# Performance work log

Measured on AMD Instinct MI355X. Metric: run time of the kernel, lower is better.

Reference implementation:

```python
import jax, jax.numpy as jnp
import numpy as np

N, E, F_IN, H, C = 50000, 800000, 50, 128, 121


def setup_inputs() -> dict:
    key = jax.random.key(0)
    ks = jax.random.split(key, 16)
    s = 0.05
    inp = {
        'x': jax.random.normal(ks[0], (N, F_IN), jnp.float32),
        'edge_index': jax.random.randint(ks[1], (2, E), 0, N, jnp.int64),
        'TRAIN': 0,
        'W1': jax.random.normal(ks[2], (F_IN, H), jnp.float32) * s,
        'b1': jnp.zeros((H,), jnp.float32),
        'W2': jax.random.normal(ks[3], (H, H), jnp.float32) * s,
        'b2': jnp.zeros((H,), jnp.float32),
        'W3': jax.random.normal(ks[4], (H, H), jnp.float32) * s,
        'b3': jnp.zeros((H,), jnp.float32),
        'fcW1': jax.random.normal(ks[5], (H, H), jnp.float32) * s,
        'fcb1': jnp.zeros((H,), jnp.float32),
        'fcW2': jax.random.normal(ks[6], (H, H), jnp.float32) * s,
        'fcb2': jnp.zeros((H,), jnp.float32),
        'fcW3': jax.random.normal(ks[7], (H, C), jnp.float32) * s,
        'fcb3': jnp.zeros((C,), jnp.float32),
    }
    return inp


def gcn_conv(x, W, b, src, dst, n):
    # PyG GCNConv: h = x @ W; symmetric norm with self-loops; aggregate at dst.
    h = x @ W
    deg = jax.ops.segment_sum(jnp.ones(src.shape[0], h.dtype), dst, num_segments=n) + 1.0
    dinv = jax.lax.rsqrt(deg)  # deg^{-1/2}, self-loop included
    norm = dinv[src] * dinv[dst]  # [E]
    agg = jax.ops.segment_sum(h[src] * norm[:, None], dst, num_segments=n)
    agg = agg + h * (dinv * dinv)[:, None]  # self-loop contribution
    return agg + b


def reference(x, edge_index, TRAIN, W1, b1, W2, b2, W3, b3, fcW1, fcb1, fcW2, fcb2, fcW3, fcb3):
    src, dst = edge_index[0], edge_index[1]
    n = x.shape[0]
    y = jax.nn.relu(gcn_conv(x, W1, b1, src, dst, n))
    y = jax.nn.relu(gcn_conv(y, W2, b2, src, dst, n))
    y = jax.nn.relu(gcn_conv(y, W3, b3, src, dst, n))
    y = jax.nn.relu(y @ fcW1 + fcb1)
    y = jax.nn.relu(y @ fcW2 + fcb2)
    y = y @ fcW3 + fcb3
    return y
```

## Files before the change

### kernel.cpp

```cpp
#include <hip/hip_runtime.h>

#define SCAN_CHUNK 2048

typedef short s16x8 __attribute__((ext_vector_type(8)));
typedef float f32x4 __attribute__((ext_vector_type(4)));

__device__ inline ushort f2b(float f) {
  uint u = __float_as_uint(f);
  return (ushort)((u + 0x7fffu + ((u >> 16) & 1u)) >> 16);
}
__device__ inline float b2f(uint h) { return __uint_as_float(h << 16); }

__global__ __launch_bounds__(256) void zero_kernel(int4* __restrict__ p, int n4) {
  int i = blockIdx.x * 256 + threadIdx.x;
  if (i < n4) p[i] = make_int4(0, 0, 0, 0);
}

__global__ __launch_bounds__(256) void convert_hist_kernel(const void* __restrict__ ei,
                                                           int* __restrict__ src,
                                                           int* __restrict__ dst,
                                                           int* __restrict__ degi, int E) {
  __shared__ int sflag;
  if (threadIdx.x == 0) {
    const int* p32 = (const int*)ei;
    int is64 = 1;
#pragma unroll 4
    for (int i = 1; i < 256; i += 2)
      if (p32[i] != 0) { is64 = 0; break; }
    sflag = is64;
  }
  __syncthreads();
  int e = blockIdx.x * 256 + threadIdx.x;
  if (e >= E) return;
  int s, d;
  if (sflag) {
    const long long* p = (const long long*)ei;
    s = (int)p[e];
    d = (int)p[E + e];
  } else {
    const int* p = (const int*)ei;
    s = p[e];
    d = p[E + e];
  }
  src[e] = s;
  dst[e] = d;
  atomicAdd(&degi[d], 1);
}

__global__ __launch_bounds__(256) void chunk_reduce_kernel(const int* __restrict__ degi,
                                                           int* __restrict__ partials, int N) {
  __shared__ int s[256];
  int base = blockIdx.x * SCAN_CHUNK;
  int sum = 0;
  for (int j = 0; j < 8; ++j) {
    int i = base + threadIdx.x * 8 + j;
    if (i < N) sum += degi[i];
  }
  s[threadIdx.x] = sum;
  __syncthreads();
  for (int ofs = 128; ofs > 0; ofs >>= 1) {
    if ((int)threadIdx.x < ofs) s[threadIdx.x] += s[threadIdx.x + ofs];
    __syncthreads();
  }
  if (threadIdx.x == 0) partials[blockIdx.x] = s[0];
}

__global__ __launch_bounds__(256) void chunk_scan_kernel(int* __restrict__ degi,
                                                         const int* __restrict__ partials,
                                                         int nchunk,
                                                         int* __restrict__ rowptr,
                                                         float* __restrict__ dinv,
                                                         int N, int E) {
  __shared__ int s[256];
  __shared__ int sbase;
  int t = threadIdx.x;
  if (t == 0) {
    int acc = 0;
    for (int c = 0; c < (int)blockIdx.x; ++c) acc += partials[c];
    sbase = acc;
    if (blockIdx.x == 0) rowptr[N] = E;
  }
  int base = blockIdx.x * SCAN_CHUNK;
  int v[8];
  int tsum = 0;
  for (int j = 0; j < 8; ++j) {
    int i = base + t * 8 + j;
    v[j] = (i < N) ? degi[i] : 0;
    tsum += v[j];
  }
  s[t] = tsum;
  __syncthreads();
  for (int ofs = 1; ofs < 256; ofs <<= 1) {
    int add = (t >= ofs) ? s[t - ofs] : 0;
    __syncthreads();
    s[t] += add;
    __syncthreads();
  }
  int run = s[t] - tsum + sbase;
  for (int j = 0; j < 8; ++j) {
    int i = base + t * 8 + j;
    if (i < N) {
      rowptr[i] = run;
      dinv[i] = rsqrtf((float)v[j] + 1.0f);
      degi[i] = 0;
    }
    run += v[j];
  }
}

__global__ __launch_bounds__(256) void scatter_kernel(const int* __restrict__ src,
                                                      const int* __restrict__ dst,
                                                      const int* __restrict__ rowptr,
                                                      const float* __restrict__ dinv,
                                                      int* __restrict__ cnt,
                                                      uint* __restrict__ epack, int E, int N) {
  const int chunk = blockIdx.x & 7;
  const int group = blockIdx.x >> 3;
  const int ngroup = gridDim.x >> 3;
  const int c0 = (int)(((long)chunk * N) >> 3);
  const int c1 = (int)(((long)(chunk + 1) * N) >> 3);
  for (int e = group * 256 + threadIdx.x; e < E; e += ngroup * 256) {
    int d = dst[e];
    if (d < c0 || d >= c1) continue;
    int s = src[e];
    int slot = rowptr[d] + atomicAdd(&cnt[d], 1);
    float nm = dinv[s] * dinv[d];
    epack[slot] = (uint)s | ((uint)f2b(nm) << 16);
  }
}

__global__ __launch_bounds__(256) void prep_all(const float* __restrict__ W1,
                                                const float* __restrict__ W2,
                                                const float* __restrict__ W3,
                                                const float* __restrict__ F1,
                                                const float* __restrict__ F2,
                                                const float* __restrict__ F3,
                                                const float* __restrict__ x,
                                                ushort* __restrict__ W1t, ushort* __restrict__ W2t,
                                                ushort* __restrict__ W3t, ushort* __restrict__ F1t,
                                                ushort* __restrict__ F2t, ushort* __restrict__ F3t,
                                                ushort* __restrict__ xb, int N) {
  int b = blockIdx.x;
  if (b < 384) {
    int wi = b >> 6;
    int i = (b & 63) * 256 + threadIdx.x;
    const float* W;
    ushort* Wt;
    int K, Kp, ncol;
    switch (wi) {
      case 0: W = W1; Wt = W1t; K = 50; Kp = 64; ncol = 128; break;
      case 1: W = W2; Wt = W2t; K = 128; Kp = 128; ncol = 128; break;
      case 2: W = W3; Wt = W3t; K = 128; Kp = 128; ncol = 128; break;
      case 3: W = F1; Wt = F1t; K = 128; Kp = 128; ncol = 128; break;
      case 4: W = F2; Wt = F2t; K = 128; Kp = 128; ncol = 128; break;
      default: W = F3; Wt = F3t; K = 128; Kp = 128; ncol = 121; break;
    }
    if (i >= 128 * Kp) return;
    int c = i / Kp, k = i - c * Kp;
    float w = (k < K && c < ncol) ? W[(size_t)k * ncol + c] : 0.f;
    Wt[(size_t)c * Kp + k] = f2b(w);
  } else {
    long i = (long)(b - 384) * 256 + threadIdx.x;
    if (i >= (long)N * 64) return;
    int n = (int)(i >> 6), k = (int)(i & 63);
    xb[i] = (k < 50) ? f2b(x[(size_t)n * 50 + k]) : (ushort)0;
  }
}

template <int KSTEPS, bool BIAS, bool RELU>
__global__ __launch_bounds__(256) void mm_mfma(const ushort* __restrict__ X,
                                               const ushort* __restrict__ Wt,
                                               const float* __restrict__ bias,
                                               ushort* __restrict__ Yb, int N) {
  constexpr int K = KSTEPS * 32;
  const int lane = threadIdx.x & 63;
  const int wq = threadIdx.x >> 6;
  const int am = lane & 15;
  const int ag = lane >> 4;

  s16x8 wf[KSTEPS][2];
#pragma unroll
  for (int ks = 0; ks < KSTEPS; ++ks)
#pragma unroll
    for (int f = 0; f < 2; ++f)
      wf[ks][f] = *(const s16x8*)(Wt + (size_t)(wq * 32 + f * 16 + am) * K + ag * 8 + ks * 32);
  float bv[2] = {0.f, 0.f};
  if (BIAS) {
    bv[0] = bias[wq * 32 + am];
    bv[1] = bias[wq * 32 + 16 + am];
  }

  const int ntile = (N + 31) >> 5;
  for (int t = blockIdx.x; t < ntile; t += gridDim.x) {
    const long r0 = (long)t * 32;
    const bool v1 = (r0 + 16) < N;
    const ushort* x0 = X + (size_t)(r0 + am) * K + ag * 8;
    f32x4 acc[2][2] = {};
#pragma unroll
    for (int ks = 0; ks < KSTEPS; ++ks) {
      s16x8 a0 = *(const s16x8*)(x0 + ks * 32);
      s16x8 a1 = {};
      if (v1) a1 = *(const s16x8*)(x0 + (size_t)16 * K + ks * 32);
#pragma unroll
      for (int f = 0; f < 2; ++f) {
        acc[0][f] = __builtin_amdgcn_mfma_f32_16x16x32_bf16(a0, wf[ks][f], acc[0][f], 0, 0, 0);
        if (v1)
          acc[1][f] = __builtin_amdgcn_mfma_f32_16x16x32_bf16(a1, wf[ks][f], acc[1][f], 0, 0, 0);
      }
    }
#pragma unroll
    for (int m = 0; m < 2; ++m) {
      if (m == 1 && !v1) break;
#pragma unroll
      for (int f = 0; f < 2; ++f) {
        int col = wq * 32 + f * 16 + am;
#pragma unroll
        for (int r = 0; r < 4; ++r) {
          long row = r0 + m * 16 + ag * 4 + r;
          float v = acc[m][f][r] + bv[f];
          if (RELU) v = fmaxf(v, 0.f);
          Yb[row * 128 + col] = f2b(v);
        }
      }
    }
  }
}

__global__ __launch_bounds__(256) void fc_fused(const ushort* __restrict__ X,
                                                const ushort* __restrict__ F1t,
                                                const ushort* __restrict__ F2t,
                                                const ushort* __restrict__ F3t,
                                                const float* __restrict__ b1,
                                                const float* __restrict__ b2,
                                                const float* __restrict__ b3,
                                                float* __restrict__ out, int N) {
  __shared__ ushort lds[32 * 128];
  const int lane = threadIdx.x & 63;
  const int wq = threadIdx.x >> 6;
  const int am = lane & 15;
  const int ag = lane >> 4;
  char* my = (char*)lds;

  s16x8 wf1[4][2], wf2[4][2], wf3[4][2];
#pragma unroll
  for (int ks = 0; ks < 4; ++ks)
#pragma unroll
    for (int f = 0; f < 2; ++f) {
      size_t o = (size_t)(wq * 32 + f * 16 + am) * 128 + ag * 8 + ks * 32;
      wf1[ks][f] = *(const s16x8*)(F1t + o);
      wf2[ks][f] = *(const s16x8*)(F2t + o);
      wf3[ks][f] = *(const s16x8*)(F3t + o);
    }
  float b1v[2] = {b1[wq * 32 + am], b1[wq * 32 + 16 + am]};
  float b2v[2] = {b2[wq * 32 + am], b2[wq * 32 + 16 + am]};
  int c0 = wq * 32 + am, c1 = wq * 32 + 16 + am;
  float b3v[2] = {(c0 < 121) ? b3[c0] : 0.f, (c1 < 121) ? b3[c1] : 0.f};

  auto stage = [&](f32x4 acc[2][2], const float* bv) {
#pragma unroll
    for (int m = 0; m < 2; ++m)
#pragma unroll
      for (int f = 0; f < 2; ++f) {
        int col = wq * 32 + f * 16 + am;
#pragma unroll
        for (int r = 0; r < 4; ++r) {
          int row = m * 16 + ag * 4 + r;
          uint byte = (uint)(row * 256 + col * 2) ^ ((uint)(row & 7) << 4);
          *(ushort*)(my + byte) = f2b(fmaxf(acc[m][f][r] + bv[f], 0.f));
        }
      }
  };
  auto loadA = [&](int m, int ks) -> s16x8 {
    int row = m * 16 + am;
    uint byte = (uint)(row * 256 + ks * 64 + ag * 16) ^ ((uint)(row & 7) << 4);
    return *(const s16x8*)(my + byte);
  };

  const int ntile = (N + 31) >> 5;
  for (int t = blockIdx.x; t < ntile; t += gridDim.x) {
    const long r0 = (long)t * 32;
    const bool v1 = (r0 + 16) < N;
    const ushort* x0 = X + (size_t)(r0 + am) * 128 + ag * 8;

    f32x4 a1c[2][2] = {};
#pragma unroll
    for (int ks = 0; ks < 4; ++ks) {
      s16x8 a0 = *(const s16x8*)(x0 + ks * 32);
      s16x8 a1 = v1 ? *(const s16x8*)(x0 + (size_t)16 * 128 + ks * 32) : s16x8{};
#pragma unroll
      for (int f = 0; f < 2; ++f) {
        a1c[0][f] = __builtin_amdgcn_mfma_f32_16x16x32_bf16(a0, wf1[ks][f], a1c[0][f], 0, 0, 0);
        a1c[1][f] = __builtin_amdgcn_mfma_f32_16x16x32_bf16(a1, wf1[ks][f], a1c[1][f], 0, 0, 0);
      }
    }
    stage(a1c, b1v);
    __syncthreads();
    f32x4 a2c[2][2] = {};
#pragma unroll
    for (int ks = 0; ks < 4; ++ks) {
      s16x8 a0 = loadA(0, ks);
      s16x8 a1 = loadA(1, ks);
#pragma unroll
      for (int f = 0; f < 2; ++f) {
        a2c[0][f] = __builtin_amdgcn_mfma_f32_16x16x32_bf16(a0, wf2[ks][f], a2c[0][f], 0, 0, 0);
        a2c[1][f] = __builtin_amdgcn_mfma_f32_16x16x32_bf16(a1, wf2[ks][f], a2c[1][f], 0, 0, 0);
      }
    }
    __syncthreads();
    stage(a2c, b2v);
    __syncthreads();
    f32x4 a3c[2][2] = {};
#pragma unroll
    for (int ks = 0; ks < 4; ++ks) {
      s16x8 a0 = loadA(0, ks);
      s16x8 a1 = loadA(1, ks);
#pragma unroll
      for (int f = 0; f < 2; ++f) {
        a3c[0][f] = __builtin_amdgcn_mfma_f32_16x16x32_bf16(a0, wf3[ks][f], a3c[0][f], 0, 0, 0);
        a3c[1][f] = __builtin_amdgcn_mfma_f32_16x16x32_bf16(a1, wf3[ks][f], a3c[1][f], 0, 0, 0);
      }
    }
#pragma unroll
    for (int m = 0; m < 2; ++m) {
      if (m == 1 && !v1) break;
#pragma unroll
      for (int f = 0; f < 2; ++f) {
        int col = wq * 32 + f * 16 + am;
        if (col >= 121) continue;
#pragma unroll
        for (int r = 0; r < 4; ++r) {
          long row = r0 + m * 16 + ag * 4 + r;
          out[row * 121 + col] = a3c[m][f][r] + b3v[f];
        }
      }
    }
    __syncthreads();
  }
}

template <int RW, bool ACT>
__global__ __launch_bounds__(256) void agg_kernel(const ushort* __restrict__ Hm,
                                                  const int* __restrict__ rowptr,
                                                  const uint* __restrict__ epack,
                                                  const float* __restrict__ dinv,
                                                  const float* __restrict__ b,
                                                  ushort* __restrict__ Y, int N) {
  int wave = threadIdx.x >> 6;
  int lane = threadIdx.x & 63;
  int n = blockIdx.x * 4 + wave;
  if (n >= N) return;
  int beg = rowptr[n], end = rowptr[n + 1];
  float dn = dinv[n];
  float d2 = dn * dn;
  int i = beg;

  if constexpr (RW == 128) {
    int f = lane * 2;
    float ax = 0.f, ay = 0.f;
    while (i + 8 <= end) {
      uint rec[8];
#pragma unroll
      for (int j = 0; j < 8; ++j) rec[j] = epack[i + j];
      uint v[8];
#pragma unroll
      for (int j = 0; j < 8; ++j)
        v[j] = *(const uint*)&Hm[(size_t)(rec[j] & 0xffffu) * 128 + f];
#pragma unroll
      for (int j = 0; j < 8; ++j) {
        float nm = __uint_as_float(rec[j] & 0xffff0000u);
        ax += b2f(v[j] & 0xffffu) * nm;
        ay += b2f(v[j] >> 16) * nm;
      }
      i += 8;
    }
    if (i + 4 <= end) {
      uint rec[4];
#pragma unroll
      for (int j = 0; j < 4; ++j) rec[j] = epack[i + j];
      uint v[4];
#pragma unroll
      for (int j = 0; j < 4; ++j)
        v[j] = *(const uint*)&Hm[(size_t)(rec[j] & 0xffffu) * 128 + f];
#pragma unroll
      for (int j = 0; j < 4; ++j) {
        float nm = __uint_as_float(rec[j] & 0xffff0000u);
        ax += b2f(v[j] & 0xffffu) * nm;
        ay += b2f(v[j] >> 16) * nm;
      }
      i += 4;
    }
    for (; i < end; ++i) {
      uint rec = epack[i];
      float nm = __uint_as_float(rec & 0xffff0000u);
      uint v = *(const uint*)&Hm[(size_t)(rec & 0xffffu) * 128 + f];
      ax += b2f(v & 0xffffu) * nm;
      ay += b2f(v >> 16) * nm;
    }
    uint sv = *(const uint*)&Hm[(size_t)n * 128 + f];
    ax += b2f(sv & 0xffffu) * d2;
    ay += b2f(sv >> 16) * d2;
    if (ACT) {
      ax = fmaxf(ax + b[f], 0.f);
      ay = fmaxf(ay + b[f + 1], 0.f);
    }
    uint out = (uint)f2b(ax) | ((uint)f2b(ay) << 16);
    *(uint*)&Y[(size_t)n * 128 + f] = out;
  } else {
    int f = lane;
    float ax = 0.f;
    while (i + 8 <= end) {
      uint rec[8];
#pragma unroll
      for (int j = 0; j < 8; ++j) rec[j] = epack[i + j];
      ushort v[8];
#pragma unroll
      for (int j = 0; j < 8; ++j)
        v[j] = Hm[(size_t)(rec[j] & 0xffffu) * 64 + f];
#pragma unroll
      for (int j = 0; j < 8; ++j)
        ax += b2f(v[j]) * __uint_as_float(rec[j] & 0xffff0000u);
      i += 8;
    }
    if (i + 4 <= end) {
      uint rec[4];
#pragma unroll
      for (int j = 0; j < 4; ++j) rec[j] = epack[i + j];
      ushort v[4];
#pragma unroll
      for (int j = 0; j < 4; ++j)
        v[j] = Hm[(size_t)(rec[j] & 0xffffu) * 64 + f];
#pragma unroll
      for (int j = 0; j < 4; ++j)
        ax += b2f(v[j]) * __uint_as_float(rec[j] & 0xffff0000u);
      i += 4;
    }
    for (; i < end; ++i) {
      uint rec = epack[i];
      ax += b2f(Hm[(size_t)(rec & 0xffffu) * 64 + f]) * __uint_as_float(rec & 0xffff0000u);
    }
    ax += b2f(Hm[(size_t)n * 64 + f]) * d2;
    if (ACT) ax = fmaxf(ax + b[f], 0.f);
    Y[(size_t)n * 64 + f] = f2b(ax);
  }
}

extern "C" void kernel_launch(void* const* d_in, const int* in_sizes, int n_in,
                              void* d_out, int out_size, void* d_ws, size_t ws_size,
                              hipStream_t stream) {
  const float* x    = (const float*)d_in[0];
  const void*  ei   = d_in[1];
  const float* W1   = (const float*)d_in[3];
  const float* b1   = (const float*)d_in[4];
  const float* W2   = (const float*)d_in[5];
  const float* b2   = (const float*)d_in[6];
  const float* W3   = (const float*)d_in[7];
  const float* b3   = (const float*)d_in[8];
  const float* fcW1 = (const float*)d_in[9];
  const float* fcb1 = (const float*)d_in[10];
  const float* fcW2 = (const float*)d_in[11];
  const float* fcb2 = (const float*)d_in[12];
  const float* fcW3 = (const float*)d_in[13];
  const float* fcb3 = (const float*)d_in[14];

  const int FIN = 50;
  const int N = in_sizes[0] / FIN;
  const int E = in_sizes[1] / 2;
  const int NCHUNK = (N + SCAN_CHUNK - 1) / SCAN_CHUNK;

  size_t off = 0;
  auto carve = [&](size_t bytes) {
    void* p = (char*)d_ws + off;
    off += (bytes + 255) & ~(size_t)255;
    return p;
  };
  int*    src32    = (int*)carve((size_t)E * 4);
  int*    dst32    = (int*)carve((size_t)E * 4);
  uint*   epack    = (uint*)carve((size_t)E * 4);
  int*    degi     = (int*)carve((size_t)(N + 4) * 4);
  int*    rowptr   = (int*)carve((size_t)(N + 1) * 4);
  float*  dinv     = (float*)carve((size_t)N * 4);
  int*    partials = (int*)carve((size_t)NCHUNK * 4);
  ushort* W1t      = (ushort*)carve((size_t)128 * 64 * 2);
  ushort* W2t      = (ushort*)carve((size_t)128 * 128 * 2);
  ushort* W3t      = (ushort*)carve((size_t)128 * 128 * 2);
  ushort* F1t      = (ushort*)carve((size_t)128 * 128 * 2);
  ushort* F2t      = (ushort*)carve((size_t)128 * 128 * 2);
  ushort* F3t      = (ushort*)carve((size_t)128 * 128 * 2);
  ushort* xb       = (ushort*)carve((size_t)N * 64 * 2);
  ushort* aggX     = (ushort*)carve((size_t)N * 64 * 2);
  ushort* bufA     = (ushort*)carve((size_t)N * 128 * 2);
  ushort* bufB     = (ushort*)carve((size_t)N * 128 * 2);

  const int gE = (E + 255) / 256;
  const int gMM = 1024;
  const int gAGG = (N + 3) / 4;
  const int gPREP = 384 + (int)(((long)N * 64 + 255) / 256);
  const int n4 = (N + 3) / 4;

  zero_kernel<<<(n4 + 255) / 256, 256, 0, stream>>>((int4*)degi, n4);
  convert_hist_kernel<<<gE, 256, 0, stream>>>(ei, src32, dst32, degi, E);
  chunk_reduce_kernel<<<NCHUNK, 256, 0, stream>>>(degi, partials, N);
  chunk_scan_kernel<<<NCHUNK, 256, 0, stream>>>(degi, partials, NCHUNK, rowptr, dinv, N, E);
  scatter_kernel<<<1024, 256, 0, stream>>>(src32, dst32, rowptr, dinv, degi, epack, E, N);
  prep_all<<<gPREP, 256, 0, stream>>>(W1, W2, W3, fcW1, fcW2, fcW3, x,
                                      W1t, W2t, W3t, F1t, F2t, F3t, xb, N);

  agg_kernel<64, false><<<gAGG, 256, 0, stream>>>(xb, rowptr, epack, dinv, nullptr, aggX, N);
  mm_mfma<2, true, true><<<gMM, 256, 0, stream>>>(aggX, W1t, b1, bufA, N);
  mm_mfma<4, false, false><<<gMM, 256, 0, stream>>>(bufA, W2t, nullptr, bufB, N);
  agg_kernel<128, true><<<gAGG, 256, 0, stream>>>(bufB, rowptr, epack, dinv, b2, bufA, N);
  mm_mfma<4, false, false><<<gMM, 256, 0, stream>>>(bufA, W3t, nullptr, bufB, N);
  agg_kernel<128, true><<<gAGG, 256, 0, stream>>>(bufB, rowptr, epack, dinv, b3, bufA, N);
  fc_fused<<<gMM, 256, 0, stream>>>(bufA, F1t, F2t, F3t, fcb1, fcb2, fcb3,
                                    (float*)d_out, N);
}
```

Baseline: 260.7 us.

## Fuse graph aggregation with following MFMA matmuls into three per-tile kernels

Replaces the separate aggregation and matmul kernels with three fused kernels. Each block gathers neighbor features for 32 rows into swizzled LDS, then applies one or more MFMA matmuls directly from LDS. This removes intermediate global round-trips (aggX, one 128-wide buffer per layer) and several launches. The zero kernel is also folded into prep_all. The cost is less latency hiding: each wave gathers 8 rows serially before a block barrier, occupancy may drop with LDS use and held weight registers, and the matmuls no longer use grid-stride tiling.

```diff
diff --git a/kernel.cpp b/kernel.cpp
--- a/kernel.cpp
+++ b/kernel.cpp
@@ -11,9 +11,123 @@
 }
 __device__ inline float b2f(uint h) { return __uint_as_float(h << 16); }
 
-__global__ __launch_bounds__(256) void zero_kernel(int4* __restrict__ p, int n4) {
-  int i = blockIdx.x * 256 + threadIdx.x;
-  if (i < n4) p[i] = make_int4(0, 0, 0, 0);
+__device__ inline void gather128(const ushort* __restrict__ Hm, const uint* __restrict__ ep,
+                                 int beg, int end, int f, float& ax, float& ay) {
+  int i = beg;
+  while (i + 8 <= end) {
+    uint rec[8];
+#pragma unroll
+    for (int j = 0; j < 8; ++j) rec[j] = ep[i + j];
+    uint v[8];
+#pragma unroll
+    for (int j = 0; j < 8; ++j) v[j] = *(const uint*)&Hm[(size_t)(rec[j] & 0xffffu) * 128 + f];
+#pragma unroll
+    for (int j = 0; j < 8; ++j) {
+      float nm = __uint_as_float(rec[j] & 0xffff0000u);
+      ax += b2f(v[j] & 0xffffu) * nm;
+      ay += b2f(v[j] >> 16) * nm;
+    }
+    i += 8;
+  }
+  if (i + 4 <= end) {
+    uint rec[4];
+#pragma unroll
+    for (int j = 0; j < 4; ++j) rec[j] = ep[i + j];
+    uint v[4];
+#pragma unroll
+    for (int j = 0; j < 4; ++j) v[j] = *(const uint*)&Hm[(size_t)(rec[j] & 0xffffu) * 128 + f];
+#pragma unroll
+    for (int j = 0; j < 4; ++j) {
+      float nm = __uint_as_float(rec[j] & 0xffff0000u);
+      ax += b2f(v[j] & 0xffffu) * nm;
+      ay += b2f(v[j] >> 16) * nm;
+    }
+    i += 4;
+  }
+  for (; i < end; ++i) {
+    uint rec = ep[i];
+    float nm = __uint_as_float(rec & 0xffff0000u);
+    uint v = *(const uint*)&Hm[(size_t)(rec & 0xffffu) * 128 + f];
+    ax += b2f(v & 0xffffu) * nm;
+    ay += b2f(v >> 16) * nm;
+  }
+}
+
+__device__ inline float gather64(const ushort* __restrict__ Hm, const uint* __restrict__ ep,
+                                 int beg, int end, int f) {
+  float ax = 0.f;
+  int i = beg;
+  while (i + 8 <= end) {
+    uint rec[8];
+#pragma unroll
+    for (int j = 0; j < 8; ++j) rec[j] = ep[i + j];
+    ushort v[8];
+#pragma unroll
+    for (int j = 0; j < 8; ++j) v[j] = Hm[(size_t)(rec[j] & 0xffffu) * 64 + f];
+#pragma unroll
+    for (int j = 0; j < 8; ++j) ax += b2f(v[j]) * __uint_as_float(rec[j] & 0xffff0000u);
+    i += 8;
+  }
+  if (i + 4 <= end) {
+    uint rec[4];
+#pragma unroll
+    for (int j = 0; j < 4; ++j) rec[j] = ep[i + j];
+    ushort v[4];
+#pragma unroll
+    for (int j = 0; j < 4; ++j) v[j] = Hm[(size_t)(rec[j] & 0xffffu) * 64 + f];
+#pragma unroll
+    for (int j = 0; j < 4; ++j) ax += b2f(v[j]) * __uint_as_float(rec[j] & 0xffff0000u);
+    i += 4;
+  }
+  for (; i < end; ++i) {
+    uint rec = ep[i];
+    ax += b2f(Hm[(size_t)(rec & 0xffffu) * 64 + f]) * __uint_as_float(rec & 0xffff0000u);
+  }
+  return ax;
+}
+
+__global__ __launch_bounds__(256) void prep_all(const float* __restrict__ W1,
+                                                const float* __restrict__ W2,
+                                                const float* __restrict__ W3,
+                                                const float* __restrict__ F1,
+                                                const float* __restrict__ F2,
+                                                const float* __restrict__ F3,
+                                                const float* __restrict__ x,
+                                                ushort* __restrict__ W1t, ushort* __restrict__ W2t,
+                                                ushort* __restrict__ W3t, ushort* __restrict__ F1t,
+                                                ushort* __restrict__ F2t, ushort* __restrict__ F3t,
+                                                ushort* __restrict__ xb, int* __restrict__ degi,
+                                                int N) {
+  const int gXB = (int)(((long)N * 64 + 255) / 256);
+  const int n4 = (N + 3) / 4;
+  int b = blockIdx.x;
+  if (b < 384) {
+    int wi = b >> 6;
+    int i = (b & 63) * 256 + threadIdx.x;
+    const float* W;
+    ushort* Wt;
+    int K, Kp, ncol;
+    switch (wi) {
+      case 0: W = W1; Wt = W1t; K = 50; Kp = 64; ncol = 128; break;
+      case 1: W = W2; Wt = W2t; K = 128; Kp = 128; ncol = 128; break;
+      case 2: W = W3; Wt = W3t; K = 128; Kp = 128; ncol = 128; break;
+      case 3: W = F1; Wt = F1t; K = 128; Kp = 128; ncol = 128; break;
+      case 4: W = F2; Wt = F2t; K = 128; Kp = 128; ncol = 128; break;
+      default: W = F3; Wt = F3t; K = 128; Kp = 128; ncol = 121; break;
+    }
+    if (i >= 128 * Kp) return;
+    int c = i / Kp, k = i - c * Kp;
+    float w = (k < K && c < ncol) ? W[(size_t)k * ncol + c] : 0.f;
+    Wt[(size_t)c * Kp + k] = f2b(w);
+  } else if (b < 384 + gXB) {
+    long i = (long)(b - 384) * 256 + threadIdx.x;
+    if (i >= (long)N * 64) return;
+    int n = (int)(i >> 6), k = (int)(i & 63);
+    xb[i] = (k < 50) ? f2b(x[(size_t)n * 50 + k]) : (ushort)0;
+  } else {
+    long i = (long)(b - 384 - gXB) * 256 + threadIdx.x;
+    if (i < n4) ((int4*)degi)[i] = make_int4(0, 0, 0, 0);
+  }
 }
 
 __global__ __launch_bounds__(256) void convert_hist_kernel(const void* __restrict__ ei,
@@ -129,318 +243,289 @@
   }
 }
 
-__global__ __launch_bounds__(256) void prep_all(const float* __restrict__ W1,
-                                                const float* __restrict__ W2,
-                                                const float* __restrict__ W3,
-                                                const float* __restrict__ F1,
-                                                const float* __restrict__ F2,
-                                                const float* __restrict__ F3,
-                                                const float* __restrict__ x,
-                                                ushort* __restrict__ W1t, ushort* __restrict__ W2t,
-                                                ushort* __restrict__ W3t, ushort* __restrict__ F1t,
-                                                ushort* __restrict__ F2t, ushort* __restrict__ F3t,
-                                                ushort* __restrict__ xb, int N) {
-  int b = blockIdx.x;
-  if (b < 384) {
-    int wi = b >> 6;
-    int i = (b & 63) * 256 + threadIdx.x;
-    const float* W;
-    ushort* Wt;
-    int K, Kp, ncol;
-    switch (wi) {
-      case 0: W = W1; Wt = W1t; K = 50; Kp = 64; ncol = 128; break;
-      case 1: W = W2; Wt = W2t; K = 128; Kp = 128; ncol = 128; break;
-      case 2: W = W3; Wt = W3t; K = 128; Kp = 128; ncol = 128; break;
-      case 3: W = F1; Wt = F1t; K = 128; Kp = 128; ncol = 128; break;
-      case 4: W = F2; Wt = F2t; K = 128; Kp = 128; ncol = 128; break;
-      default: W = F3; Wt = F3t; K = 128; Kp = 128; ncol = 121; break;
-    }
-    if (i >= 128 * Kp) return;
-    int c = i / Kp, k = i - c * Kp;
-    float w = (k < K && c < ncol) ? W[(size_t)k * ncol + c] : 0.f;
-    Wt[(size_t)c * Kp + k] = f2b(w);
-  } else {
-    long i = (long)(b - 384) * 256 + threadIdx.x;
-    if (i >= (long)N * 64) return;
-    int n = (int)(i >> 6), k = (int)(i & 63);
-    xb[i] = (k < 50) ? f2b(x[(size_t)n * 50 + k]) : (ushort)0;
-  }
-}
-
-template <int KSTEPS, bool BIAS, bool RELU>
-__global__ __launch_bounds__(256) void mm_mfma(const ushort* __restrict__ X,
-                                               const ushort* __restrict__ Wt,
-                                               const float* __restrict__ bias,
-                                               ushort* __restrict__ Yb, int N) {
-  constexpr int K = KSTEPS * 32;
+__global__ __launch_bounds__(256) void fusedA(const ushort* __restrict__ xb,
+                                              const int* __restrict__ rowptr,
+                                              const uint* __restrict__ epack,
+                                              const float* __restrict__ dinv,
+                                              const ushort* __restrict__ W1t,
+                                              const ushort* __restrict__ W2t,
+                                              const float* __restrict__ b1,
+                                              ushort* __restrict__ h2, int N) {
+  __shared__ char lds[4096 + 8192];
   const int lane = threadIdx.x & 63;
-  const int wq = threadIdx.x >> 6;
-  const int am = lane & 15;
-  const int ag = lane >> 4;
-
-  s16x8 wf[KSTEPS][2];
-#pragma unroll
-  for (int ks = 0; ks < KSTEPS; ++ks)
+  const int w = threadIdx.x >> 6;
+  const int am = lane & 15, ag = lane >> 4;
+
+  s16x8 wf1[2][2], wf2[4][2];
+#pragma unroll
+  for (int ks = 0; ks < 2; ++ks)
 #pragma unroll
     for (int f = 0; f < 2; ++f)
-      wf[ks][f] = *(const s16x8*)(Wt + (size_t)(wq * 32 + f * 16 + am) * K + ag * 8 + ks * 32);
-  float bv[2] = {0.f, 0.f};
-  if (BIAS) {
-    bv[0] = bias[wq * 32 + am];
-    bv[1] = bias[wq * 32 + 16 + am];
-  }
-
-  const int ntile = (N + 31) >> 5;
-  for (int t = blockIdx.x; t < ntile; t += gridDim.x) {
-    const long r0 = (long)t * 32;
-    const bool v1 = (r0 + 16) < N;
-    const ushort* x0 = X + (size_t)(r0 + am) * K + ag * 8;
-    f32x4 acc[2][2] = {};
-#pragma unroll
-    for (int ks = 0; ks < KSTEPS; ++ks) {
-      s16x8 a0 = *(const s16x8*)(x0 + ks * 32);
-      s16x8 a1 = {};
-      if (v1) a1 = *(const s16x8*)(x0 + (size_t)16 * K + ks * 32);
-#pragma unroll
-      for (int f = 0; f < 2; ++f) {
-        acc[0][f] = __builtin_amdgcn_mfma_f32_16x16x32_bf16(a0, wf[ks][f], acc[0][f], 0, 0, 0);
-        if (v1)
-          acc[1][f] = __builtin_amdgcn_mfma_f32_16x16x32_bf16(a1, wf[ks][f], acc[1][f], 0, 0, 0);
+      wf1[ks][f] = *(const s16x8*)(W1t + (size_t)(w * 32 + f * 16 + am) * 64 + ks * 32 + ag * 8);
+#pragma unroll
+  for (int ks = 0; ks < 4; ++ks)
+#pragma unroll
+    for (int f = 0; f < 2; ++f)
+      wf2[ks][f] = *(const s16x8*)(W2t + (size_t)(w * 32 + f * 16 + am) * 128 + ks * 32 + ag * 8);
+  float b1v[2] = {b1[w * 32 + am], b1[w * 32 + 16 + am]};
+
+  const long r0 = (long)blockIdx.x * 32;
+  for (int j = 0; j < 8; ++j) {
+    int row = w * 8 + j;
+    long n = r0 + row;
+    float ax = 0.f;
+    if (n < N) {
+      ax = gather64(xb, epack, rowptr[n], rowptr[n + 1], lane);
+      float dn = dinv[n];
+      ax += b2f(xb[(size_t)n * 64 + lane]) * (dn * dn);
+    }
+    uint byte = (uint)(row * 128 + lane * 2) ^ ((uint)(row & 7) << 4);
+    *(ushort*)(lds + byte) = f2b(ax);
+  }
+  __syncthreads();
+  f32x4 a1c[2][2] = {};
+#pragma unroll
+  for (int ks = 0; ks < 2; ++ks) {
+    int rA = am, rB = 16 + am;
+    s16x8 a0 = *(const s16x8*)(lds + (((uint)(rA * 128 + ks * 64 + ag * 16)) ^ ((uint)(rA & 7) << 4)));
+    s16x8 a1 = *(const s16x8*)(lds + (((uint)(rB * 128 + ks * 64 + ag * 16)) ^ ((uint)(rB & 7) << 4)));
+#pragma unroll
+    for (int f = 0; f < 2; ++f) {
+      a1c[0][f] = __builtin_amdgcn_mfma_f32_16x16x32_bf16(a0, wf1[ks][f], a1c[0][f], 0, 0, 0);
+      a1c[1][f] = __builtin_amdgcn_mfma_f32_16x16x32_bf16(a1, wf1[ks][f], a1c[1][f], 0, 0, 0);
+    }
+  }
+#pragma unroll
+  for (int m = 0; m < 2; ++m)
+#pragma unroll
+    for (int f = 0; f < 2; ++f) {
+      int col = w * 32 + f * 16 + am;
+#pragma unroll
+      for (int r = 0; r < 4; ++r) {
+        int row = m * 16 + ag * 4 + r;
+        uint byte = 4096u + (((uint)(row * 256 + col * 2)) ^ ((uint)(row & 7) << 4));
+        *(ushort*)(lds + byte) = f2b(fmaxf(a1c[m][f][r] + b1v[f], 0.f));
       }
     }
-#pragma unroll
-    for (int m = 0; m < 2; ++m) {
-      if (m == 1 && !v1) break;
-#pragma unroll
-      for (int f = 0; f < 2; ++f) {
-        int col = wq * 32 + f * 16 + am;
-#pragma unroll
-        for (int r = 0; r < 4; ++r) {
-          long row = r0 + m * 16 + ag * 4 + r;
-          float v = acc[m][f][r] + bv[f];
-          if (RELU) v = fmaxf(v, 0.f);
-          Yb[row * 128 + col] = f2b(v);
-        }
+  __syncthreads();
+  f32x4 a2c[2][2] = {};
+#pragma unroll
+  for (int ks = 0; ks < 4; ++ks) {
+    int rA = am, rB = 16 + am;
+    s16x8 a0 = *(const s16x8*)(lds + 4096u + (((uint)(rA * 256 + ks * 64 + ag * 16)) ^ ((uint)(rA & 7) << 4)));
+    s16x8 a1 = *(const s16x8*)(lds + 4096u + (((uint)(rB * 256 + ks * 64 + ag * 16)) ^ ((uint)(rB & 7) << 4)));
+#pragma unroll
+    for (int f = 0; f < 2; ++f) {
+      a2c[0][f] = __builtin_amdgcn_mfma_f32_16x16x32_bf16(a0, wf2[ks][f], a2c[0][f], 0, 0, 0);
+      a2c[1][f] = __builtin_amdgcn_mfma_f32_16x16x32_bf16(a1, wf2[ks][f], a2c[1][f], 0, 0, 0);
+    }
+  }
+  const bool v1 = (r0 + 16) < N;
+#pragma unroll
+  for (int m = 0; m < 2; ++m) {
+    if (m == 1 && !v1) break;
+#pragma unroll
+    for (int f = 0; f < 2; ++f) {
+      int col = w * 32 + f * 16 + am;
+#pragma unroll
+      for (int r = 0; r < 4; ++r) {
+        long row = r0 + m * 16 + ag * 4 + r;
+        h2[row * 128 + col] = f2b(a2c[m][f][r]);
       }
     }
   }
 }
 
-__global__ __launch_bounds__(256) void fc_fused(const ushort* __restrict__ X,
-                                                const ushort* __restrict__ F1t,
-                                                const ushort* __restrict__ F2t,
-                                                const ushort* __restrict__ F3t,
-                                                const float* __restrict__ b1,
-                                                const float* __restrict__ b2,
-                                                const float* __restrict__ b3,
-                                                float* __restrict__ out, int N) {
-  __shared__ ushort lds[32 * 128];
+__global__ __launch_bounds__(256) void fusedB(const ushort* __restrict__ Hin,
+                                              const int* __restrict__ rowptr,
+                                              const uint* __restrict__ epack,
+                                              const float* __restrict__ dinv,
+                                              const ushort* __restrict__ Wt,
+                                              const float* __restrict__ bagg,
+                                              ushort* __restrict__ Hout, int N) {
+  __shared__ char lds[8192];
   const int lane = threadIdx.x & 63;
-  const int wq = threadIdx.x >> 6;
-  const int am = lane & 15;
-  const int ag = lane >> 4;
-  char* my = (char*)lds;
+  const int w = threadIdx.x >> 6;
+  const int am = lane & 15, ag = lane >> 4;
+
+  s16x8 wf[4][2];
+#pragma unroll
+  for (int ks = 0; ks < 4; ++ks)
+#pragma unroll
+    for (int f = 0; f < 2; ++f)
+      wf[ks][f] = *(const s16x8*)(Wt + (size_t)(w * 32 + f * 16 + am) * 128 + ks * 32 + ag * 8);
+  float blo = bagg[lane * 2], bhi = bagg[lane * 2 + 1];
+
+  const long r0 = (long)blockIdx.x * 32;
+  for (int j = 0; j < 8; ++j) {
+    int row = w * 8 + j;
+    long n = r0 + row;
+    float ax = 0.f, ay = 0.f;
+    if (n < N) {
+      gather128(Hin, epack, rowptr[n], rowptr[n + 1], lane * 2, ax, ay);
+      float dn = dinv[n];
+      float d2 = dn * dn;
+      uint sv = *(const uint*)&Hin[(size_t)n * 128 + lane * 2];
+      ax = fmaxf(ax + b2f(sv & 0xffffu) * d2 + blo, 0.f);
+      ay = fmaxf(ay + b2f(sv >> 16) * d2 + bhi, 0.f);
+    }
+    uint pk = (uint)f2b(ax) | ((uint)f2b(ay) << 16);
+    uint byte = (uint)(row * 256 + lane * 4) ^ ((uint)(row & 7) << 4);
+    *(uint*)(lds + byte) = pk;
+  }
+  __syncthreads();
+  f32x4 acc[2][2] = {};
+#pragma unroll
+  for (int ks = 0; ks < 4; ++ks) {
+    int rA = am, rB = 16 + am;
+    s16x8 a0 = *(const s16x8*)(lds + (((uint)(rA * 256 + ks * 64 + ag * 16)) ^ ((uint)(rA & 7) << 4)));
+    s16x8 a1 = *(const s16x8*)(lds + (((uint)(rB * 256 + ks * 64 + ag * 16)) ^ ((uint)(rB & 7) << 4)));
+#pragma unroll
+    for (int f = 0; f < 2; ++f) {
+      acc[0][f] = __builtin_amdgcn_mfma_f32_16x16x32_bf16(a0, wf[ks][f], acc[0][f], 0, 0, 0);
+      acc[1][f] = __builtin_amdgcn_mfma_f32_16x16x32_bf16(a1, wf[ks][f], acc[1][f], 0, 0, 0);
+    }
+  }
+  const bool v1 = (r0 + 16) < N;
+#pragma unroll
+  for (int m = 0; m < 2; ++m) {
+    if (m == 1 && !v1) break;
+#pragma unroll
+    for (int f = 0; f < 2; ++f) {
+      int col = w * 32 + f * 16 + am;
+#pragma unroll
+      for (int r = 0; r < 4; ++r) {
+        long row = r0 + m * 16 + ag * 4 + r;
+        Hout[row * 128 + col] = f2b(acc[m][f][r]);
+      }
+    }
+  }
+}
+
+__global__ __launch_bounds__(256) void fusedC(const ushort* __restrict__ Hin,
+                                              const int* __restrict__ rowptr,
+                                              const uint* __restrict__ epack,
+                                              const float* __restrict__ dinv,
+                                              const ushort* __restrict__ F1t,
+                                              const ushort* __restrict__ F2t,
+                                              const ushort* __restrict__ F3t,
+                                              const float* __restrict__ bagg,
+                                              const float* __restrict__ fb1,
+                                              const float* __restrict__ fb2,
+                                              const float* __restrict__ fb3,
+                                              float* __restrict__ out, int N) {
+  __shared__ char lds[8192];
+  const int lane = threadIdx.x & 63;
+  const int w = threadIdx.x >> 6;
+  const int am = lane & 15, ag = lane >> 4;
 
   s16x8 wf1[4][2], wf2[4][2], wf3[4][2];
 #pragma unroll
   for (int ks = 0; ks < 4; ++ks)
 #pragma unroll
     for (int f = 0; f < 2; ++f) {
-      size_t o = (size_t)(wq * 32 + f * 16 + am) * 128 + ag * 8 + ks * 32;
+      size_t o = (size_t)(w * 32 + f * 16 + am) * 128 + ks * 32 + ag * 8;
       wf1[ks][f] = *(const s16x8*)(F1t + o);
       wf2[ks][f] = *(const s16x8*)(F2t + o);
       wf3[ks][f] = *(const s16x8*)(F3t + o);
     }
-  float b1v[2] = {b1[wq * 32 + am], b1[wq * 32 + 16 + am]};
-  float b2v[2] = {b2[wq * 32 + am], b2[wq * 32 + 16 + am]};
-  int c0 = wq * 32 + am, c1 = wq * 32 + 16 + am;
-  float b3v[2] = {(c0 < 121) ? b3[c0] : 0.f, (c1 < 121) ? b3[c1] : 0.f};
-
+  float blo = bagg[lane * 2], bhi = bagg[lane * 2 + 1];
+  float fb1v[2] = {fb1[w * 32 + am], fb1[w * 32 + 16 + am]};
+  float fb2v[2] = {fb2[w * 32 + am], fb2[w * 32 + 16 + am]};
+  int c0 = w * 32 + am, c1 = w * 32 + 16 + am;
+  float fb3v[2] = {(c0 < 121) ? fb3[c0] : 0.f, (c1 < 121) ? fb3[c1] : 0.f};
+
+  auto loadA = [&](int m, int ks) -> s16x8 {
+    int row = m * 16 + am;
+    uint byte = (uint)(row * 256 + ks * 64 + ag * 16) ^ ((uint)(row & 7) << 4);
+    return *(const s16x8*)(lds + byte);
+  };
   auto stage = [&](f32x4 acc[2][2], const float* bv) {
 #pragma unroll
     for (int m = 0; m < 2; ++m)
 #pragma unroll
       for (int f = 0; f < 2; ++f) {
-        int col = wq * 32 + f * 16 + am;
+        int col = w * 32 + f * 16 + am;
 #pragma unroll
         for (int r = 0; r < 4; ++r) {
           int row = m * 16 + ag * 4 + r;
           uint byte = (uint)(row * 256 + col * 2) ^ ((uint)(row & 7) << 4);
-          *(ushort*)(my + byte) = f2b(fmaxf(acc[m][f][r] + bv[f], 0.f));
+          *(ushort*)(lds + byte) = f2b(fmaxf(acc[m][f][r] + bv[f], 0.f));
         }
       }
   };
-  auto loadA = [&](int m, int ks) -> s16x8 {
-    int row = m * 16 + am;
-    uint byte = (uint)(row * 256 + ks * 64 + ag * 16) ^ ((uint)(row & 7) << 4);
-    return *(const s16x8*)(my + byte);
-  };
-
-  const int ntile = (N + 31) >> 5;
-  for (int t = blockIdx.x; t < ntile; t += gridDim.x) {
-    const long r0 = (long)t * 32;
-    const bool v1 = (r0 + 16) < N;
-    const ushort* x0 = X + (size_t)(r0 + am) * 128 + ag * 8;
-
-    f32x4 a1c[2][2] = {};
-#pragma unroll
-    for (int ks = 0; ks < 4; ++ks) {
-      s16x8 a0 = *(const s16x8*)(x0 + ks * 32);
-      s16x8 a1 = v1 ? *(const s16x8*)(x0 + (size_t)16 * 128 + ks * 32) : s16x8{};
-#pragma unroll
-      for (int f = 0; f < 2; ++f) {
-        a1c[0][f] = __builtin_amdgcn_mfma_f32_16x16x32_bf16(a0, wf1[ks][f], a1c[0][f], 0, 0, 0);
-        a1c[1][f] = __builtin_amdgcn_mfma_f32_16x16x32_bf16(a1, wf1[ks][f], a1c[1][f], 0, 0, 0);
+
+  const long r0 = (long)blockIdx.x * 32;
+  for (int j = 0; j < 8; ++j) {
+    int row = w * 8 + j;
+    long n = r0 + row;
+    float ax = 0.f, ay = 0.f;
+    if (n < N) {
+      gather128(Hin, epack, rowptr[n], rowptr[n + 1], lane * 2, ax, ay);
+      float dn = dinv[n];
+      float d2 = dn * dn;
+      uint sv = *(const uint*)&Hin[(size_t)n * 128 + lane * 2];
+      ax = fmaxf(ax + b2f(sv & 0xffffu) * d2 + blo, 0.f);
+      ay = fmaxf(ay + b2f(sv >> 16) * d2 + bhi, 0.f);
+    }
+    uint pk = (uint)f2b(ax) | ((uint)f2b(ay) << 16);
+    uint byte = (uint)(row * 256 + lane * 4) ^ ((uint)(row & 7) << 4);
+    *(uint*)(lds + byte) = pk;
+  }
+  __syncthreads();
+  f32x4 a1c[2][2] = {};
+#pragma unroll
+  for (int ks = 0; ks < 4; ++ks) {
+    s16x8 a0 = loadA(0, ks);
+    s16x8 a1 = loadA(1, ks);
+#pragma unroll
+    for (int f = 0; f < 2; ++f) {
+      a1c[0][f] = __builtin_amdgcn_mfma_f32_16x16x32_bf16(a0, wf1[ks][f], a1c[0][f], 0, 0, 0);
+      a1c[1][f] = __builtin_amdgcn_mfma_f32_16x16x32_bf16(a1, wf1[ks][f], a1c[1][f], 0, 0, 0);
+    }
+  }
+  __syncthreads();
+  stage(a1c, fb1v);
+  __syncthreads();
+  f32x4 a2c[2][2] = {};
+#pragma unroll
+  for (int ks = 0; ks < 4; ++ks) {
+    s16x8 a0 = loadA(0, ks);
+    s16x8 a1 = loadA(1, ks);
+#pragma unroll
+    for (int f = 0; f < 2; ++f) {
+      a2c[0][f] = __builtin_amdgcn_mfma_f32_16x16x32_bf16(a0, wf2[ks][f], a2c[0][f], 0, 0, 0);
+      a2c[1][f] = __builtin_amdgcn_mfma_f32_16x16x32_bf16(a1, wf2[ks][f], a2c[1][f], 0, 0, 0);
+    }
+  }
+  __syncthreads();
+  stage(a2c, fb2v);
+  __syncthreads();
+  f32x4 a3c[2][2] = {};
+#pragma unroll
+  for (int ks = 0; ks < 4; ++ks) {
+    s16x8 a0 = loadA(0, ks);
+    s16x8 a1 = loadA(1, ks);
+#pragma unroll
+    for (int f = 0; f < 2; ++f) {
+      a3c[0][f] = __builtin_amdgcn_mfma_f32_16x16x32_bf16(a0, wf3[ks][f], a3c[0][f], 0, 0, 0);
+      a3c[1][f] = __builtin_amdgcn_mfma_f32_16x16x32_bf16(a1, wf3[ks][f], a3c[1][f], 0, 0, 0);
+    }
+  }
+  const bool v1 = (r0 + 16) < N;
+#pragma unroll
+  for (int m = 0; m < 2; ++m) {
+    if (m == 1 && !v1) break;
+#pragma unroll
+    for (int f = 0; f < 2; ++f) {
+      int col = w * 32 + f * 16 + am;
+      if (col >= 121) continue;
+#pragma unroll
+      for (int r = 0; r < 4; ++r) {
+        long row = r0 + m * 16 + ag * 4 + r;
+        out[row * 121 + col] = a3c[m][f][r] + fb3v[f];
       }
     }
-    stage(a1c, b1v);
-    __syncthreads();
-    f32x4 a2c[2][2] = {};
-#pragma unroll
-    for (int ks = 0; ks < 4; ++ks) {
-      s16x8 a0 = loadA(0, ks);
-      s16x8 a1 = loadA(1, ks);
-#pragma unroll
-      for (int f = 0; f < 2; ++f) {
-        a2c[0][f] = __builtin_amdgcn_mfma_f32_16x16x32_bf16(a0, wf2[ks][f], a2c[0][f], 0, 0, 0);
-        a2c[1][f] = __builtin_amdgcn_mfma_f32_16x16x32_bf16(a1, wf2[ks][f], a2c[1][f], 0, 0, 0);
-      }
-    }
-    __syncthreads();
-    stage(a2c, b2v);
-    __syncthreads();
-    f32x4 a3c[2][2] = {};
-#pragma unroll
-    for (int ks = 0; ks < 4; ++ks) {
-      s16x8 a0 = loadA(0, ks);
-      s16x8 a1 = loadA(1, ks);
-#pragma unroll
-      for (int f = 0; f < 2; ++f) {
-        a3c[0][f] = __builtin_amdgcn_mfma_f32_16x16x32_bf16(a0, wf3[ks][f], a3c[0][f], 0, 0, 0);
-        a3c[1][f] = __builtin_amdgcn_mfma_f32_16x16x32_bf16(a1, wf3[ks][f], a3c[1][f], 0, 0, 0);
-      }
-    }
-#pragma unroll
-    for (int m = 0; m < 2; ++m) {
-      if (m == 1 && !v1) break;
-#pragma unroll
-      for (int f = 0; f < 2; ++f) {
-        int col = wq * 32 + f * 16 + am;
-        if (col >= 121) continue;
-#pragma unroll
-        for (int r = 0; r < 4; ++r) {
-          long row = r0 + m * 16 + ag * 4 + r;
-          out[row * 121 + col] = a3c[m][f][r] + b3v[f];
-        }
-      }
-    }
-    __syncthreads();
-  }
-}
-
-template <int RW, bool ACT>
-__global__ __launch_bounds__(256) void agg_kernel(const ushort* __restrict__ Hm,
-                                                  const int* __restrict__ rowptr,
-                                                  const uint* __restrict__ epack,
-                                                  const float* __restrict__ dinv,
-                                                  const float* __restrict__ b,
-                                                  ushort* __restrict__ Y, int N) {
-  int wave = threadIdx.x >> 6;
-  int lane = threadIdx.x & 63;
-  int n = blockIdx.x * 4 + wave;
-  if (n >= N) return;
-  int beg = rowptr[n], end = rowptr[n + 1];
-  float dn = dinv[n];
-  float d2 = dn * dn;
-  int i = beg;
-
-  if constexpr (RW == 128) {
-    int f = lane * 2;
-    float ax = 0.f, ay = 0.f;
-    while (i + 8 <= end) {
-      uint rec[8];
-#pragma unroll
-      for (int j = 0; j < 8; ++j) rec[j] = epack[i + j];
-      uint v[8];
-#pragma unroll
-      for (int j = 0; j < 8; ++j)
-        v[j] = *(const uint*)&Hm[(size_t)(rec[j] & 0xffffu) * 128 + f];
-#pragma unroll
-      for (int j = 0; j < 8; ++j) {
-        float nm = __uint_as_float(rec[j] & 0xffff0000u);
-        ax += b2f(v[j] & 0xffffu) * nm;
-        ay += b2f(v[j] >> 16) * nm;
-      }
-      i += 8;
-    }
-    if (i + 4 <= end) {
-      uint rec[4];
-#pragma unroll
-      for (int j = 0; j < 4; ++j) rec[j] = epack[i + j];
-      uint v[4];
-#pragma unroll
-      for (int j = 0; j < 4; ++j)
-        v[j] = *(const uint*)&Hm[(size_t)(rec[j] & 0xffffu) * 128 + f];
-#pragma unroll
-      for (int j = 0; j < 4; ++j) {
-        float nm = __uint_as_float(rec[j] & 0xffff0000u);
-        ax += b2f(v[j] & 0xffffu) * nm;
-        ay += b2f(v[j] >> 16) * nm;
-      }
-      i += 4;
-    }
-    for (; i < end; ++i) {
-      uint rec = epack[i];
-      float nm = __uint_as_float(rec & 0xffff0000u);
-      uint v = *(const uint*)&Hm[(size_t)(rec & 0xffffu) * 128 + f];
-      ax += b2f(v & 0xffffu) * nm;
-      ay += b2f(v >> 16) * nm;
-    }
-    uint sv = *(const uint*)&Hm[(size_t)n * 128 + f];
-    ax += b2f(sv & 0xffffu) * d2;
-    ay += b2f(sv >> 16) * d2;
-    if (ACT) {
-      ax = fmaxf(ax + b[f], 0.f);
-      ay = fmaxf(ay + b[f + 1], 0.f);
-    }
-    uint out = (uint)f2b(ax) | ((uint)f2b(ay) << 16);
-    *(uint*)&Y[(size_t)n * 128 + f] = out;
-  } else {
-    int f = lane;
-    float ax = 0.f;
-    while (i + 8 <= end) {
-      uint rec[8];
-#pragma unroll
-      for (int j = 0; j < 8; ++j) rec[j] = epack[i + j];
-      ushort v[8];
-#pragma unroll
-      for (int j = 0; j < 8; ++j)
-        v[j] = Hm[(size_t)(rec[j] & 0xffffu) * 64 + f];
-#pragma unroll
-      for (int j = 0; j < 8; ++j)
-        ax += b2f(v[j]) * __uint_as_float(rec[j] & 0xffff0000u);
-      i += 8;
-    }
-    if (i + 4 <= end) {
-      uint rec[4];
-#pragma unroll
-      for (int j = 0; j < 4; ++j) rec[j] = epack[i + j];
-      ushort v[4];
-#pragma unroll
-      for (int j = 0; j < 4; ++j)
-        v[j] = Hm[(size_t)(rec[j] & 0xffffu) * 64 + f];
-#pragma unroll
-      for (int j = 0; j < 4; ++j)
-        ax += b2f(v[j]) * __uint_as_float(rec[j] & 0xffff0000u);
-      i += 4;
-    }
-    for (; i < end; ++i) {
-      uint rec = epack[i];
-      ax += b2f(Hm[(size_t)(rec & 0xffffu) * 64 + f]) * __uint_as_float(rec & 0xffff0000u);
-    }
-    ax += b2f(Hm[(size_t)n * 64 + f]) * d2;
-    if (ACT) ax = fmaxf(ax + b[f], 0.f);
-    Y[(size_t)n * 64 + f] = f2b(ax);
   }
 }
 
@@ -487,30 +572,24 @@
   ushort* F2t      = (ushort*)carve((size_t)128 * 128 * 2);
   ushort* F3t      = (ushort*)carve((size_t)128 * 128 * 2);
   ushort* xb       = (ushort*)carve((size_t)N * 64 * 2);
-  ushort* aggX     = (ushort*)carve((size_t)N * 64 * 2);
   ushort* bufA     = (ushort*)carve((size_t)N * 128 * 2);
   ushort* bufB     = (ushort*)carve((size_t)N * 128 * 2);
 
   const int gE = (E + 255) / 256;
-  const int gMM = 1024;
-  const int gAGG = (N + 3) / 4;
-  const int gPREP = 384 + (int)(((long)N * 64 + 255) / 256);
+  const int NT = (N + 31) / 32;
+  const int gXB = (int)(((long)N * 64 + 255) / 256);
   const int n4 = (N + 3) / 4;
-
-  zero_kernel<<<(n4 + 255) / 256, 256, 0, stream>>>((int4*)degi, n4);
+  const int gZ = (n4 + 255) / 256;
+
+  prep_all<<<384 + gXB + gZ, 256, 0, stream>>>(W1, W2, W3, fcW1, fcW2, fcW3, x,
+                                               W1t, W2t, W3t, F1t, F2t, F3t, xb, degi, N);
   convert_hist_kernel<<<gE, 256, 0, stream>>>(ei, src32, dst32, degi, E);
   chunk_reduce_kernel<<<NCHUNK, 256, 0, stream>>>(degi, partials, N);
   chunk_scan_kernel<<<NCHUNK, 256, 0, stream>>>(degi, partials, NCHUNK, rowptr, dinv, N, E);
   scatter_kernel<<<1024, 256, 0, stream>>>(src32, dst32, rowptr, dinv, degi, epack, E, N);
-  prep_all<<<gPREP, 256, 0, stream>>>(W1, W2, W3, fcW1, fcW2, fcW3, x,
-                                      W1t, W2t, W3t, F1t, F2t, F3t, xb, N);
-
-  agg_kernel<64, false><<<gAGG, 256, 0, stream>>>(xb, rowptr, epack, dinv, nullptr, aggX, N);
-  mm_mfma<2, true, true><<<gMM, 256, 0, stream>>>(aggX, W1t, b1, bufA, N);
-  mm_mfma<4, false, false><<<gMM, 256, 0, stream>>>(bufA, W2t, nullptr, bufB, N);
-  agg_kernel<128, true><<<gAGG, 256, 0, stream>>>(bufB, rowptr, epack, dinv, b2, bufA, N);
-  mm_mfma<4, false, false><<<gMM, 256, 0, stream>>>(bufA, W3t, nullptr, bufB, N);
-  agg_kernel<128, true><<<gAGG, 256, 0, stream>>>(bufB, rowptr, epack, dinv, b3, bufA, N);
-  fc_fused<<<gMM, 256, 0, stream>>>(bufA, F1t, F2t, F3t, fcb1, fcb2, fcb3,
-                                    (float*)d_out, N);
-}
+
+  fusedA<<<NT, 256, 0, stream>>>(xb, rowptr, epack, dinv, W1t, W2t, b1, bufB, N);
+  fusedB<<<NT, 256, 0, stream>>>(bufB, rowptr, epack, dinv, W3t, b2, bufA, N);
+  fusedC<<<NT, 256, 0, stream>>>(bufA, rowptr, epack, dinv, F1t, F2t, F3t,
+                                 b3, fcb1, fcb2, fcb3, (float*)d_out, N);
+}
```

New measurement: 339.6 us. 1.3x slower.
